# Kernel tuning notes

Measured on AMD Instinct MI355X. Metric: run time of the kernel, lower is better.

The kernel has to match this reference:

```python
import jax, jax.numpy as jnp
import numpy as np

N_NODES = 50000
N_EDGES = 800000
HID = 64
F_NODE = 64
F_EDGE = 16
DEC_H = 64
EPS = 1e-5


def setup_inputs() -> dict:
    key = jax.random.key(0)
    ks = jax.random.split(key, 16)
    inp = {}
    inp['x'] = jax.random.normal(ks[0], (N_NODES, F_NODE), dtype=jnp.float32)
    inp['edge_index'] = jax.random.randint(ks[1], (2, N_EDGES), 0, N_NODES, dtype=jnp.int32)
    inp['edge_attr'] = jax.random.normal(ks[2], (N_EDGES, F_EDGE), dtype=jnp.float32)
    # 3 GCN layers (F_NODE == HID so weights stack)
    inp['conv_w'] = jax.random.normal(ks[3], (3, HID, HID), dtype=jnp.float32) / np.sqrt(HID)
    inp['conv_b'] = jnp.zeros((3, HID), dtype=jnp.float32)
    inp['ln_g'] = jnp.ones((3, HID), dtype=jnp.float32)
    inp['ln_b'] = jnp.zeros((3, HID), dtype=jnp.float32)
    dec_in = 2 * HID + F_EDGE
    inp['dec_w1'] = jax.random.normal(ks[4], (dec_in, DEC_H), dtype=jnp.float32) / np.sqrt(dec_in)
    inp['dec_b1'] = jnp.zeros((DEC_H,), dtype=jnp.float32)
    inp['dec_w2'] = jax.random.normal(ks[5], (DEC_H, DEC_H // 2), dtype=jnp.float32) / np.sqrt(DEC_H)
    inp['dec_b2'] = jnp.zeros((DEC_H // 2,), dtype=jnp.float32)
    inp['dec_w3'] = jax.random.normal(ks[6], (DEC_H // 2, 1), dtype=jnp.float32) / np.sqrt(DEC_H // 2)
    inp['dec_b3'] = jnp.zeros((1,), dtype=jnp.float32)
    return inp


def _layer_norm(h, g, b):
    mu = jnp.mean(h, axis=-1, keepdims=True)
    var = jnp.mean(jnp.square(h - mu), axis=-1, keepdims=True)
    return (h - mu) * jax.lax.rsqrt(var + EPS) * g + b


def _forward(x, edge_index, edge_attr, conv_w, conv_b, ln_g, ln_b,
             dec_w1, dec_b1, dec_w2, dec_b2, dec_w3, dec_b3):
    n = x.shape[0]
    src, dst = edge_index[0], edge_index[1]
    # add self-loops (PyG GCNConv default)
    loop = jnp.arange(n, dtype=edge_index.dtype)
    src_sl = jnp.concatenate([src, loop])
    dst_sl = jnp.concatenate([dst, loop])
    # symmetric normalization: deg over target column (incl. self-loops)
    deg = jax.ops.segment_sum(jnp.ones_like(src_sl, dtype=x.dtype), dst_sl, num_segments=n)
    dinv = jnp.where(deg > 0, jax.lax.rsqrt(deg), 0.0)
    norm = dinv[src_sl] * dinv[dst_sl]  # (E+N,)

    h = x
    for l in range(conv_w.shape[0]):
        t = h @ conv_w[l]                                   # (N, H)
        msg = t[src_sl] * norm[:, None]                     # (E+N, H)
        agg = jax.ops.segment_sum(msg, dst_sl, num_segments=n) + conv_b[l]
        h = jax.nn.relu(_layer_norm(agg, ln_g[l], ln_b[l]))
        # dropout is identity at inference

    # edge decoder: concat(src_emb, dst_emb, edge_attr) -> MLP -> scalar
    z = jnp.concatenate([h[src], h[dst], edge_attr], axis=-1)  # (E, 2H+Fe)
    z = jax.nn.relu(z @ dec_w1 + dec_b1)
    z = jax.nn.relu(z @ dec_w2 + dec_b2)
    return (z @ dec_w3 + dec_b3).squeeze(-1)                   # (E,)


def reference(x, edge_index, edge_attr, conv_w, conv_b, ln_g, ln_b,
              dec_w1, dec_b1, dec_w2, dec_b2, dec_w3, dec_b3):
    return _forward(x, edge_index, edge_attr, conv_w, conv_b, ln_g, ln_b,
                    dec_w1, dec_b1, dec_w2, dec_b2, dec_w3, dec_b3)
```

## Files before the change

kernel.cpp:

```cpp
#include <hip/hip_runtime.h>
#include <hip/hip_fp16.h>

#define N_NODES 50000
#define N_EDGES 800000
#define HID 64
#define F_EDGE 16
#define LN_EPS 1e-5f
#define SCAN_BLOCKS ((N_NODES + 255) / 256)

typedef _Float16 h2n __attribute__((ext_vector_type(2)));

__device__ inline h2n to_n(__half2 v) {
    union { __half2 a; h2n b; } u; u.a = v; return u.b;
}
__device__ inline h2n pack2(float x, float y) {
    h2n r; r.x = (_Float16)x; r.y = (_Float16)y; return r;
}

__device__ inline float wave_sum64(float v) {
    #pragma unroll
    for (int o = 32; o > 0; o >>= 1) v += __shfl_xor(v, o, 64);
    return v;
}

__global__ void k_zero_cnt(int* __restrict__ cnt) {
    int i = blockIdx.x * blockDim.x + threadIdx.x;
    if (i < N_NODES) cnt[i] = 0;
}

__global__ void k_count(const int* __restrict__ dst, int* __restrict__ cnt) {
    int e = blockIdx.x * blockDim.x + threadIdx.x;
    if (e < N_EDGES) atomicAdd(&cnt[dst[e]], 1);
}

__global__ void k_scan1(const int* __restrict__ cnt, int* __restrict__ row_ptr,
                        int* __restrict__ bsum, float* __restrict__ dinv) {
    __shared__ int wsum[4];
    int tid = threadIdx.x, lane = tid & 63, w = tid >> 6;
    int i = blockIdx.x * 256 + tid;
    int v = (i < N_NODES) ? cnt[i] : 0;
    if (i < N_NODES) dinv[i] = rsqrtf((float)v + 1.0f);
    int isc = v;
    #pragma unroll
    for (int o = 1; o < 64; o <<= 1) {
        int n = __shfl_up(isc, o, 64);
        if (lane >= o) isc += n;
    }
    if (lane == 63) wsum[w] = isc;
    __syncthreads();
    int woff = 0;
    #pragma unroll
    for (int k = 0; k < 4; k++) woff += (k < w) ? wsum[k] : 0;
    if (i < N_NODES) row_ptr[i] = woff + isc - v;
    if (tid == 255) bsum[blockIdx.x] = woff + isc;
}

__global__ void k_scan2_prep(const int* __restrict__ bsum, int* __restrict__ boff,
                             const float* __restrict__ W1c, const float* __restrict__ W2,
                             __half2* __restrict__ w1cp, __half2* __restrict__ w2p) {
    __shared__ int wsum[4];
    int tid = threadIdx.x, lane = tid & 63, w = tid >> 6;
    int v = (tid < SCAN_BLOCKS) ? bsum[tid] : 0;
    int isc = v;
    #pragma unroll
    for (int o = 1; o < 64; o <<= 1) {
        int n = __shfl_up(isc, o, 64);
        if (lane >= o) isc += n;
    }
    if (lane == 63) wsum[w] = isc;
    __syncthreads();
    int woff = 0;
    #pragma unroll
    for (int k = 0; k < 4; k++) woff += (k < w) ? wsum[k] : 0;
    if (tid < SCAN_BLOCKS) boff[tid] = woff + isc - v;
    for (int i = tid; i < 8 * 64; i += 256) {
        int k2 = i >> 6, j = i & 63;
        w1cp[i] = __floats2half2_rn(W1c[(2 * k2) * 64 + j], W1c[(2 * k2 + 1) * 64 + j]);
    }
    for (int i = tid; i < 32 * 32; i += 256) {
        int k2 = i >> 5, j = i & 31;
        w2p[i] = __floats2half2_rn(W2[(2 * k2) * 32 + j], W2[(2 * k2 + 1) * 32 + j]);
    }
}

__global__ void k_scan3(int* __restrict__ row_ptr, const int* __restrict__ boff,
                        int* __restrict__ cursor) {
    int i = blockIdx.x * blockDim.x + threadIdx.x;
    if (i < N_NODES) {
        int r = row_ptr[i] + boff[i >> 8];
        row_ptr[i] = r;
        cursor[i] = r;
    }
    if (i == 0) row_ptr[N_NODES] = N_EDGES;
}

__global__ void k_fill(const int* __restrict__ src, const int* __restrict__ dst,
                       int* __restrict__ cursor, int* __restrict__ col) {
    int e = blockIdx.x * blockDim.x + threadIdx.x;
    if (e < N_EDGES) {
        int s = src[e], d = dst[e];
        int pos = atomicAdd(&cursor[d], 1);
        col[pos] = s;
    }
}

__global__ void k_xs_init(const float* __restrict__ x, const float* __restrict__ dinv,
                          __half* __restrict__ xs) {
    int i = blockIdx.x * blockDim.x + threadIdx.x;
    if (i < N_NODES * 64) xs[i] = __float2half_rn(x[i] * dinv[i >> 6]);
}

__global__ void __launch_bounds__(256)
k_gather_agg(const __half* __restrict__ xs, const float* __restrict__ dinv,
             const int* __restrict__ row_ptr, const int* __restrict__ col,
             float* __restrict__ agg) {
    int gid = blockIdx.x * blockDim.x + threadIdx.x;
    int wid = gid >> 6, lane = gid & 63;
    int nA = wid * 2;
    if (nA >= N_NODES) return;
    nA = __builtin_amdgcn_readfirstlane(nA);
    int nB = nA + 1;
    int q = lane >> 3;
    int c8 = lane & 7;
    const float4* x4 = (const float4*)xs;

    float accA[8], accB[8];
    #pragma unroll
    for (int u = 0; u < 8; u++) { accA[u] = 0.0f; accB[u] = 0.0f; }

    if (q == 0) {
        float4 raw = x4[(size_t)nA * 8 + c8];
        const __half2* hp = (const __half2*)&raw;
        float2 f0 = __half22float2(hp[0]);
        float2 f1 = __half22float2(hp[1]);
        float2 f2 = __half22float2(hp[2]);
        float2 f3 = __half22float2(hp[3]);
        accA[0] = f0.x; accA[1] = f0.y; accA[2] = f1.x; accA[3] = f1.y;
        accA[4] = f2.x; accA[5] = f2.y; accA[6] = f3.x; accA[7] = f3.y;
    } else if (q == 1) {
        float4 raw = x4[(size_t)nB * 8 + c8];
        const __half2* hp = (const __half2*)&raw;
        float2 f0 = __half22float2(hp[0]);
        float2 f1 = __half22float2(hp[1]);
        float2 f2 = __half22float2(hp[2]);
        float2 f3 = __half22float2(hp[3]);
        accB[0] = f0.x; accB[1] = f0.y; accB[2] = f1.x; accB[3] = f1.y;
        accB[4] = f2.x; accB[5] = f2.y; accB[6] = f3.x; accB[7] = f3.y;
    }

    int begA = row_ptr[nA];
    int begB = row_ptr[nA + 1];
    int endB = row_ptr[nA + 2];
    int degA = begB - begA;
    int degB = endB - begB;

    int cLA = 0, cLB = 0;
    if (lane < degA) cLA = col[begA + lane];
    if (lane < degB) cLB = col[begB + lane];
    int stepsA = (min(degA, 64) + 7) >> 3;
    int stepsB = (min(degB, 64) + 7) >> 3;
    int steps = max(stepsA, stepsB);

    #pragma unroll 2
    for (int st = 0; st < steps; st++) {
        int idx = 8 * st + q;
        int sA = __shfl(cLA, idx, 64);
        int sB = __shfl(cLB, idx, 64);
        float mA = (idx < degA) ? 1.0f : 0.0f;
        float mB = (idx < degB) ? 1.0f : 0.0f;
        float4 rA = x4[(size_t)sA * 8 + c8];
        float4 rB = x4[(size_t)sB * 8 + c8];
        const __half2* ha = (const __half2*)&rA;
        const __half2* hb = (const __half2*)&rB;
        float2 a0 = __half22float2(ha[0]), a1 = __half22float2(ha[1]);
        float2 a2 = __half22float2(ha[2]), a3 = __half22float2(ha[3]);
        float2 b0 = __half22float2(hb[0]), b1 = __half22float2(hb[1]);
        float2 b2 = __half22float2(hb[2]), b3 = __half22float2(hb[3]);
        accA[0] = fmaf(a0.x, mA, accA[0]); accA[1] = fmaf(a0.y, mA, accA[1]);
        accA[2] = fmaf(a1.x, mA, accA[2]); accA[3] = fmaf(a1.y, mA, accA[3]);
        accA[4] = fmaf(a2.x, mA, accA[4]); accA[5] = fmaf(a2.y, mA, accA[5]);
        accA[6] = fmaf(a3.x, mA, accA[6]); accA[7] = fmaf(a3.y, mA, accA[7]);
        accB[0] = fmaf(b0.x, mB, accB[0]); accB[1] = fmaf(b0.y, mB, accB[1]);
        accB[2] = fmaf(b1.x, mB, accB[2]); accB[3] = fmaf(b1.y, mB, accB[3]);
        accB[4] = fmaf(b2.x, mB, accB[4]); accB[5] = fmaf(b2.y, mB, accB[5]);
        accB[6] = fmaf(b3.x, mB, accB[6]); accB[7] = fmaf(b3.y, mB, accB[7]);
    }
    for (int j = begA + 64 + q; j < begB; j += 8) {
        int s = col[j];
        float4 raw = x4[(size_t)s * 8 + c8];
        const __half2* hp = (const __half2*)&raw;
        float2 f0 = __half22float2(hp[0]), f1 = __half22float2(hp[1]);
        float2 f2 = __half22float2(hp[2]), f3 = __half22float2(hp[3]);
        accA[0] += f0.x; accA[1] += f0.y; accA[2] += f1.x; accA[3] += f1.y;
        accA[4] += f2.x; accA[5] += f2.y; accA[6] += f3.x; accA[7] += f3.y;
    }
    for (int j = begB + 64 + q; j < endB; j += 8) {
        int s = col[j];
        float4 raw = x4[(size_t)s * 8 + c8];
        const __half2* hp = (const __half2*)&raw;
        float2 f0 = __half22float2(hp[0]), f1 = __half22float2(hp[1]);
        float2 f2 = __half22float2(hp[2]), f3 = __half22float2(hp[3]);
        accB[0] += f0.x; accB[1] += f0.y; accB[2] += f1.x; accB[3] += f1.y;
        accB[4] += f2.x; accB[5] += f2.y; accB[6] += f3.x; accB[7] += f3.y;
    }

    #pragma unroll
    for (int o = 8; o <= 32; o <<= 1) {
        #pragma unroll
        for (int u = 0; u < 8; u++) {
            accA[u] += __shfl_xor(accA[u], o, 64);
            accB[u] += __shfl_xor(accB[u], o, 64);
        }
    }

    if (q == 0) {
        float di = dinv[nA];
        float4 y0, y1;
        y0.x = accA[0] * di; y0.y = accA[1] * di; y0.z = accA[2] * di; y0.w = accA[3] * di;
        y1.x = accA[4] * di; y1.y = accA[5] * di; y1.z = accA[6] * di; y1.w = accA[7] * di;
        float4* a4 = (float4*)agg;
        a4[(size_t)nA * 16 + 2 * c8] = y0;
        a4[(size_t)nA * 16 + 2 * c8 + 1] = y1;
    } else if (q == 1) {
        float di = dinv[nB];
        float4 y0, y1;
        y0.x = accB[0] * di; y0.y = accB[1] * di; y0.z = accB[2] * di; y0.w = accB[3] * di;
        y1.x = accB[4] * di; y1.y = accB[5] * di; y1.z = accB[6] * di; y1.w = accB[7] * di;
        float4* a4 = (float4*)agg;
        a4[(size_t)nB * 16 + 2 * c8] = y0;
        a4[(size_t)nB * 16 + 2 * c8 + 1] = y1;
    }
}

__global__ void __launch_bounds__(256)
k_gemm_ln(const float* __restrict__ agg, const float* __restrict__ W,
          const float* __restrict__ cb, const float* __restrict__ g,
          const float* __restrict__ b, const float* __restrict__ dinv,
          __half* __restrict__ xs_out, float* __restrict__ h_out) {
    int lane = threadIdx.x & 63;
    int wid = (blockIdx.x * blockDim.x + threadIdx.x) >> 6;
    int nwaves = (gridDim.x * blockDim.x) >> 6;
    float w[64];
    #pragma unroll
    for (int k = 0; k < 64; k++) w[k] = W[k * 64 + lane];
    float cbl = cb[lane], gl = g[lane], bl = b[lane];
    for (int row = wid; row < N_NODES; row += nwaves) {
        int r = __builtin_amdgcn_readfirstlane(row);
        const float* xr = agg + r * 64;
        float acc = cbl;
        #pragma unroll
        for (int k = 0; k < 64; k++) acc = fmaf(xr[k], w[k], acc);
        float mu = wave_sum64(acc) * (1.0f / 64.0f);
        float d = acc - mu;
        float var = wave_sum64(d * d) * (1.0f / 64.0f);
        float y = fmaxf(fmaf(d * rsqrtf(var + LN_EPS), gl, bl), 0.0f);
        if (xs_out) {
            xs_out[r * 64 + lane] = __float2half_rn(y * dinv[r]);
        } else {
            h_out[r * 64 + lane] = y;
        }
    }
}

__global__ void __launch_bounds__(256)
k_gemm_pq(const float* __restrict__ hin, const float* __restrict__ Wp,
          const float* __restrict__ bp, const float* __restrict__ Wq,
          __half* __restrict__ P, __half* __restrict__ Q) {
    int half_g = gridDim.x >> 1;
    bool isQ = (blockIdx.x >= half_g);
    const float* W = isQ ? Wq : Wp;
    __half* out = isQ ? Q : P;
    int lane = threadIdx.x & 63;
    int bid = isQ ? (blockIdx.x - half_g) : blockIdx.x;
    int wid = (bid * blockDim.x + threadIdx.x) >> 6;
    int nwaves = (half_g * blockDim.x) >> 6;
    float w[64];
    #pragma unroll
    for (int k = 0; k < 64; k++) w[k] = W[k * 64 + lane];
    float binit = isQ ? 0.0f : bp[lane];
    for (int row = wid; row < N_NODES; row += nwaves) {
        int r = __builtin_amdgcn_readfirstlane(row);
        const float* xr = hin + r * 64;
        float acc = binit;
        #pragma unroll
        for (int k = 0; k < 64; k++) acc = fmaf(xr[k], w[k], acc);
        out[r * 64 + lane] = __float2half_rn(acc);
    }
}

__global__ void __launch_bounds__(256)
k_decoder(const __half* __restrict__ P, const __half* __restrict__ Q,
          const int* __restrict__ src, const int* __restrict__ dst,
          const float* __restrict__ attr,
          const __half2* __restrict__ w1cp,
          const __half2* __restrict__ w2p, const float* __restrict__ b2,
          const float* __restrict__ W3, const float* __restrict__ b3,
          float* __restrict__ out) {
    int e = blockIdx.x * blockDim.x + threadIdx.x;
    if (e >= N_EDGES) return;
    int s = src[e], d = dst[e];

    const float4* ap = (const float4*)(attr + (size_t)e * 16);
    float4 av0 = ap[0], av1 = ap[1], av2 = ap[2], av3 = ap[3];
    h2n a2[8];
    a2[0] = pack2(av0.x, av0.y); a2[1] = pack2(av0.z, av0.w);
    a2[2] = pack2(av1.x, av1.y); a2[3] = pack2(av1.z, av1.w);
    a2[4] = pack2(av2.x, av2.y); a2[5] = pack2(av2.z, av2.w);
    a2[6] = pack2(av3.x, av3.y); a2[7] = pack2(av3.z, av3.w);

    float acc[64];
    const float4* Pp = (const float4*)(P + (size_t)s * 64);
    const float4* Qp = (const float4*)(Q + (size_t)d * 64);
    #pragma unroll
    for (int c = 0; c < 8; c++) {
        float4 pv = Pp[c], qv = Qp[c];
        const __half2* ph = (const __half2*)&pv;
        const __half2* qh = (const __half2*)&qv;
        #pragma unroll
        for (int u = 0; u < 4; u++) {
            float2 pf = __half22float2(ph[u]);
            float2 qf = __half22float2(qh[u]);
            acc[8 * c + 2 * u]     = pf.x + qf.x;
            acc[8 * c + 2 * u + 1] = pf.y + qf.y;
        }
    }

    #pragma unroll
    for (int k2 = 0; k2 < 8; k2++) {
        #pragma unroll
        for (int j = 0; j < 64; j++)
            acc[j] = __builtin_amdgcn_fdot2(a2[k2], to_n(w1cp[k2 * 64 + j]), acc[j], false);
    }

    h2n hh[32];
    #pragma unroll
    for (int k2 = 0; k2 < 32; k2++)
        hh[k2] = pack2(fmaxf(acc[2 * k2], 0.0f), fmaxf(acc[2 * k2 + 1], 0.0f));

    float acc2[32];
    #pragma unroll
    for (int j = 0; j < 32; j++) acc2[j] = b2[j];
    #pragma unroll
    for (int k2 = 0; k2 < 32; k2++) {
        #pragma unroll
        for (int j = 0; j < 32; j++)
            acc2[j] = __builtin_amdgcn_fdot2(hh[k2], to_n(w2p[k2 * 32 + j]), acc2[j], false);
    }

    float o = b3[0];
    #pragma unroll
    for (int j = 0; j < 32; j++)
        o = fmaf(fmaxf(acc2[j], 0.0f), W3[j], o);
    out[e] = o;
}

extern "C" void kernel_launch(void* const* d_in, const int* in_sizes, int n_in,
                              void* d_out, int out_size, void* d_ws, size_t ws_size,
                              hipStream_t stream) {
    const float* x      = (const float*)d_in[0];
    const int*   ei     = (const int*)d_in[1];
    const float* attr   = (const float*)d_in[2];
    const float* conv_w = (const float*)d_in[3];
    const float* conv_b = (const float*)d_in[4];
    const float* ln_g   = (const float*)d_in[5];
    const float* ln_b   = (const float*)d_in[6];
    const float* dw1    = (const float*)d_in[7];
    const float* db1    = (const float*)d_in[8];
    const float* dw2    = (const float*)d_in[9];
    const float* db2    = (const float*)d_in[10];
    const float* dw3    = (const float*)d_in[11];
    const float* db3    = (const float*)d_in[12];
    float* out = (float*)d_out;

    const int* src = ei;
    const int* dst = ei + N_EDGES;

    char* p = (char*)d_ws;
    float*   dinv    = (float*)p;   p += sizeof(float) * N_NODES;
    float*   agg     = (float*)p;   p += sizeof(float) * (size_t)N_NODES * 64;
    float*   h3      = (float*)p;   p += sizeof(float) * (size_t)N_NODES * 64;
    __half*  xs      = (__half*)p;  p += sizeof(__half) * (size_t)N_NODES * 64;
    __half*  P_h     = (__half*)p;  p += sizeof(__half) * (size_t)N_NODES * 64;
    __half*  Q_h     = (__half*)p;  p += sizeof(__half) * (size_t)N_NODES * 64;
    int*     cnt     = (int*)p;     p += sizeof(int) * N_NODES;
    int*     cursor  = (int*)p;     p += sizeof(int) * N_NODES;
    int*     row_ptr = (int*)p;     p += sizeof(int) * (N_NODES + 1);
    int*     col     = (int*)p;     p += sizeof(int) * N_EDGES;
    int*     bsum    = (int*)p;     p += sizeof(int) * 256;
    int*     boff    = (int*)p;     p += sizeof(int) * 256;
    __half2* w1cp    = (__half2*)p; p += sizeof(__half2) * 8 * 64;
    __half2* w2p     = (__half2*)p; p += sizeof(__half2) * 32 * 32;

    const int nb_nodes = (N_NODES + 255) / 256;
    const int nb_edges = (N_EDGES + 255) / 256;
    const int nb_elems = (N_NODES * 64 + 255) / 256;

    k_zero_cnt<<<nb_nodes, 256, 0, stream>>>(cnt);
    k_count<<<nb_edges, 256, 0, stream>>>(dst, cnt);
    k_scan1<<<SCAN_BLOCKS, 256, 0, stream>>>(cnt, row_ptr, bsum, dinv);
    k_scan2_prep<<<1, 256, 0, stream>>>(bsum, boff, dw1 + 128 * 64, dw2, w1cp, w2p);
    k_scan3<<<nb_nodes, 256, 0, stream>>>(row_ptr, boff, cursor);
    k_fill<<<nb_edges, 256, 0, stream>>>(src, dst, cursor, col);
    k_xs_init<<<nb_elems, 256, 0, stream>>>(x, dinv, xs);

    const int gemm_blocks = 1024;
    const int gather_blocks = N_NODES / 8;

    for (int l = 0; l < 3; l++) {
        k_gather_agg<<<gather_blocks, 256, 0, stream>>>(xs, dinv, row_ptr, col, agg);
        bool last = (l == 2);
        k_gemm_ln<<<gemm_blocks, 256, 0, stream>>>(
            agg, conv_w + l * 4096, conv_b + l * 64,
            ln_g + l * 64, ln_b + l * 64, dinv,
            last ? (__half*)nullptr : xs, last ? h3 : (float*)nullptr);
    }

    k_gemm_pq<<<2 * gemm_blocks, 256, 0, stream>>>(h3, dw1, db1, dw1 + 64 * 64, P_h, Q_h);

    k_decoder<<<nb_edges, 256, 0, stream>>>(
        P_h, Q_h, src, dst, attr, w1cp, w2p, db2, dw3, db3, out);
}
```

Measured before the change: 449.2 us.

## Assign eight lanes per node in gather-aggregate with software-pipelined neighbor loads

The gather kernel no longer gives two nodes to each 64-lane wave and splitting neighbors across lane groups. It now uses 8 lanes per node, so a wave covers 8 nodes. Each group walks its node's neighbor list serially, four neighbors at a time, and prefetches the next four column indices while the current rows load. This removes the cross-lane shuffle reduction and the idle lanes on low-degree nodes. The cost is serial per-node latency and load imbalance within a wave when node degrees differ.

```diff
diff --git a/kernel.cpp b/kernel.cpp
--- a/kernel.cpp
+++ b/kernel.cpp
@@ -110,126 +110,79 @@
     if (i < N_NODES * 64) xs[i] = __float2half_rn(x[i] * dinv[i >> 6]);
 }
 
+__device__ inline void row_acc(float4 raw, float m, float acc[8]) {
+    const __half2* hp = (const __half2*)&raw;
+    float2 f0 = __half22float2(hp[0]);
+    float2 f1 = __half22float2(hp[1]);
+    float2 f2 = __half22float2(hp[2]);
+    float2 f3 = __half22float2(hp[3]);
+    acc[0] = fmaf(f0.x, m, acc[0]); acc[1] = fmaf(f0.y, m, acc[1]);
+    acc[2] = fmaf(f1.x, m, acc[2]); acc[3] = fmaf(f1.y, m, acc[3]);
+    acc[4] = fmaf(f2.x, m, acc[4]); acc[5] = fmaf(f2.y, m, acc[5]);
+    acc[6] = fmaf(f3.x, m, acc[6]); acc[7] = fmaf(f3.y, m, acc[7]);
+}
+
 __global__ void __launch_bounds__(256)
 k_gather_agg(const __half* __restrict__ xs, const float* __restrict__ dinv,
              const int* __restrict__ row_ptr, const int* __restrict__ col,
              float* __restrict__ agg) {
     int gid = blockIdx.x * blockDim.x + threadIdx.x;
-    int wid = gid >> 6, lane = gid & 63;
-    int nA = wid * 2;
-    if (nA >= N_NODES) return;
-    nA = __builtin_amdgcn_readfirstlane(nA);
-    int nB = nA + 1;
-    int q = lane >> 3;
-    int c8 = lane & 7;
+    int n = gid >> 3;
+    if (n >= N_NODES) return;
+    int c8 = gid & 7;
     const float4* x4 = (const float4*)xs;
 
-    float accA[8], accB[8];
-    #pragma unroll
-    for (int u = 0; u < 8; u++) { accA[u] = 0.0f; accB[u] = 0.0f; }
-
-    if (q == 0) {
-        float4 raw = x4[(size_t)nA * 8 + c8];
+    float acc[8];
+    {
+        float4 raw = x4[(size_t)n * 8 + c8];
         const __half2* hp = (const __half2*)&raw;
         float2 f0 = __half22float2(hp[0]);
         float2 f1 = __half22float2(hp[1]);
         float2 f2 = __half22float2(hp[2]);
         float2 f3 = __half22float2(hp[3]);
-        accA[0] = f0.x; accA[1] = f0.y; accA[2] = f1.x; accA[3] = f1.y;
-        accA[4] = f2.x; accA[5] = f2.y; accA[6] = f3.x; accA[7] = f3.y;
-    } else if (q == 1) {
-        float4 raw = x4[(size_t)nB * 8 + c8];
-        const __half2* hp = (const __half2*)&raw;
-        float2 f0 = __half22float2(hp[0]);
-        float2 f1 = __half22float2(hp[1]);
-        float2 f2 = __half22float2(hp[2]);
-        float2 f3 = __half22float2(hp[3]);
-        accB[0] = f0.x; accB[1] = f0.y; accB[2] = f1.x; accB[3] = f1.y;
-        accB[4] = f2.x; accB[5] = f2.y; accB[6] = f3.x; accB[7] = f3.y;
-    }
-
-    int begA = row_ptr[nA];
-    int begB = row_ptr[nA + 1];
-    int endB = row_ptr[nA + 2];
-    int degA = begB - begA;
-    int degB = endB - begB;
-
-    int cLA = 0, cLB = 0;
-    if (lane < degA) cLA = col[begA + lane];
-    if (lane < degB) cLB = col[begB + lane];
-    int stepsA = (min(degA, 64) + 7) >> 3;
-    int stepsB = (min(degB, 64) + 7) >> 3;
-    int steps = max(stepsA, stepsB);
-
-    #pragma unroll 2
-    for (int st = 0; st < steps; st++) {
-        int idx = 8 * st + q;
-        int sA = __shfl(cLA, idx, 64);
-        int sB = __shfl(cLB, idx, 64);
-        float mA = (idx < degA) ? 1.0f : 0.0f;
-        float mB = (idx < degB) ? 1.0f : 0.0f;
-        float4 rA = x4[(size_t)sA * 8 + c8];
-        float4 rB = x4[(size_t)sB * 8 + c8];
-        const __half2* ha = (const __half2*)&rA;
-        const __half2* hb = (const __half2*)&rB;
-        float2 a0 = __half22float2(ha[0]), a1 = __half22float2(ha[1]);
-        float2 a2 = __half22float2(ha[2]), a3 = __half22float2(ha[3]);
-        float2 b0 = __half22float2(hb[0]), b1 = __half22float2(hb[1]);
-        float2 b2 = __half22float2(hb[2]), b3 = __half22float2(hb[3]);
-        accA[0] = fmaf(a0.x, mA, accA[0]); accA[1] = fmaf(a0.y, mA, accA[1]);
-        accA[2] = fmaf(a1.x, mA, accA[2]); accA[3] = fmaf(a1.y, mA, accA[3]);
-        accA[4] = fmaf(a2.x, mA, accA[4]); accA[5] = fmaf(a2.y, mA, accA[5]);
-        accA[6] = fmaf(a3.x, mA, accA[6]); accA[7] = fmaf(a3.y, mA, accA[7]);
-        accB[0] = fmaf(b0.x, mB, accB[0]); accB[1] = fmaf(b0.y, mB, accB[1]);
-        accB[2] = fmaf(b1.x, mB, accB[2]); accB[3] = fmaf(b1.y, mB, accB[3]);
-        accB[4] = fmaf(b2.x, mB, accB[4]); accB[5] = fmaf(b2.y, mB, accB[5]);
-        accB[6] = fmaf(b3.x, mB, accB[6]); accB[7] = fmaf(b3.y, mB, accB[7]);
-    }
-    for (int j = begA + 64 + q; j < begB; j += 8) {
-        int s = col[j];
-        float4 raw = x4[(size_t)s * 8 + c8];
-        const __half2* hp = (const __half2*)&raw;
-        float2 f0 = __half22float2(hp[0]), f1 = __half22float2(hp[1]);
-        float2 f2 = __half22float2(hp[2]), f3 = __half22float2(hp[3]);
-        accA[0] += f0.x; accA[1] += f0.y; accA[2] += f1.x; accA[3] += f1.y;
-        accA[4] += f2.x; accA[5] += f2.y; accA[6] += f3.x; accA[7] += f3.y;
-    }
-    for (int j = begB + 64 + q; j < endB; j += 8) {
-        int s = col[j];
-        float4 raw = x4[(size_t)s * 8 + c8];
-        const __half2* hp = (const __half2*)&raw;
-        float2 f0 = __half22float2(hp[0]), f1 = __half22float2(hp[1]);
-        float2 f2 = __half22float2(hp[2]), f3 = __half22float2(hp[3]);
-        accB[0] += f0.x; accB[1] += f0.y; accB[2] += f1.x; accB[3] += f1.y;
-        accB[4] += f2.x; accB[5] += f2.y; accB[6] += f3.x; accB[7] += f3.y;
-    }
-
-    #pragma unroll
-    for (int o = 8; o <= 32; o <<= 1) {
-        #pragma unroll
-        for (int u = 0; u < 8; u++) {
-            accA[u] += __shfl_xor(accA[u], o, 64);
-            accB[u] += __shfl_xor(accB[u], o, 64);
+        acc[0] = f0.x; acc[1] = f0.y; acc[2] = f1.x; acc[3] = f1.y;
+        acc[4] = f2.x; acc[5] = f2.y; acc[6] = f3.x; acc[7] = f3.y;
+    }
+
+    int beg = row_ptr[n], end = row_ptr[n + 1];
+    int t = beg;
+    int s0 = 0, s1 = 0, s2 = 0, s3 = 0;
+    if (t < end) {
+        int e1 = end - 1;
+        s0 = col[t];
+        s1 = col[min(t + 1, e1)];
+        s2 = col[min(t + 2, e1)];
+        s3 = col[min(t + 3, e1)];
+    }
+    while (t < end) {
+        float m1 = (t + 1 < end) ? 1.0f : 0.0f;
+        float m2 = (t + 2 < end) ? 1.0f : 0.0f;
+        float m3 = (t + 3 < end) ? 1.0f : 0.0f;
+        float4 r0 = x4[(size_t)s0 * 8 + c8];
+        float4 r1 = x4[(size_t)s1 * 8 + c8];
+        float4 r2 = x4[(size_t)s2 * 8 + c8];
+        float4 r3 = x4[(size_t)s3 * 8 + c8];
+        t += 4;
+        if (t < end) {
+            int e1 = end - 1;
+            s0 = col[t];
+            s1 = col[min(t + 1, e1)];
+            s2 = col[min(t + 2, e1)];
+            s3 = col[min(t + 3, e1)];
         }
-    }
-
-    if (q == 0) {
-        float di = dinv[nA];
-        float4 y0, y1;
-        y0.x = accA[0] * di; y0.y = accA[1] * di; y0.z = accA[2] * di; y0.w = accA[3] * di;
-        y1.x = accA[4] * di; y1.y = accA[5] * di; y1.z = accA[6] * di; y1.w = accA[7] * di;
-        float4* a4 = (float4*)agg;
-        a4[(size_t)nA * 16 + 2 * c8] = y0;
-        a4[(size_t)nA * 16 + 2 * c8 + 1] = y1;
-    } else if (q == 1) {
-        float di = dinv[nB];
-        float4 y0, y1;
-        y0.x = accB[0] * di; y0.y = accB[1] * di; y0.z = accB[2] * di; y0.w = accB[3] * di;
-        y1.x = accB[4] * di; y1.y = accB[5] * di; y1.z = accB[6] * di; y1.w = accB[7] * di;
-        float4* a4 = (float4*)agg;
-        a4[(size_t)nB * 16 + 2 * c8] = y0;
-        a4[(size_t)nB * 16 + 2 * c8 + 1] = y1;
-    }
+        row_acc(r0, 1.0f, acc);
+        row_acc(r1, m1, acc);
+        row_acc(r2, m2, acc);
+        row_acc(r3, m3, acc);
+    }
+
+    float di = dinv[n];
+    float4 y0, y1;
+    y0.x = acc[0] * di; y0.y = acc[1] * di; y0.z = acc[2] * di; y0.w = acc[3] * di;
+    y1.x = acc[4] * di; y1.y = acc[5] * di; y1.z = acc[6] * di; y1.w = acc[7] * di;
+    float4* a4 = (float4*)agg;
+    a4[(size_t)n * 16 + 2 * c8] = y0;
+    a4[(size_t)n * 16 + 2 * c8 + 1] = y1;
 }
 
 __global__ void __launch_bounds__(256)
@@ -404,7 +357,7 @@
     k_xs_init<<<nb_elems, 256, 0, stream>>>(x, dinv, xs);
 
     const int gemm_blocks = 1024;
-    const int gather_blocks = N_NODES / 8;
+    const int gather_blocks = (N_NODES * 8 + 255) / 256;
 
     for (int l = 0; l < 3; l++) {
         k_gather_agg<<<gather_blocks, 256, 0, stream>>>(xs, dinv, row_ptr, col, agg);
```

Result: faster. 438.8 us (-2.3%).
